# Kernel tuning notes

Hardware: AMD Instinct MI355X
Metric: run time of the kernel (lower is better)

Reference implementation:

```python
import jax, jax.numpy as jnp
import numpy as np
from jax import lax

N_T, N_CAPS, CAP_DIM = 8, 16, 16
EPS = 1e-6


def setup_inputs() -> dict:
    key = jax.random.key(0)
    k1, k2 = jax.random.split(key)
    B, H, W = 4, 64, 64
    C = N_T * N_CAPS * CAP_DIM  # 2048
    z = jax.random.normal(k1, (B, C, H, W), dtype=jnp.float32)
    u = jax.random.normal(k2, (B, C, H, W), dtype=jnp.float32)
    weight = jnp.ones((1, 1, 3, 3, 1), dtype=jnp.float32)  # Conv3d (O,I,kT,kD,kS), init ones
    beta = jnp.ones((1,), dtype=jnp.float32)  # correlated_mean_beta, mu_init=1.0
    return {"z": z, "u": u, "weight": weight, "beta": beta}


def reference(z, u, weight, beta):
    B, C, H, W = u.shape
    hw = H * W
    # (B, n_t, n_caps, cap_dim, hw) -> (B, n_caps, n_t, cap_dim, hw) -> (B*n_caps, 1, n_t, cap_dim, hw)
    u_caps = u.reshape(B, N_T, N_CAPS, CAP_DIM, hw)
    u_caps = jnp.transpose(u_caps, (0, 2, 1, 3, 4))
    u_caps = u_caps.reshape(-1, 1, N_T, CAP_DIM, hw)
    u_sq = u_caps * u_caps
    # circular pad over transform and cap_dim axes to keep 'same' size with 3x3x1 kernel
    padded = jnp.pad(u_sq, ((0, 0), (0, 0), (1, 1), (1, 1), (0, 0)), mode="wrap")
    v = lax.conv_general_dilated(
        padded, weight, window_strides=(1, 1, 1), padding="VALID",
        dimension_numbers=("NCDHW", "OIDHW", "NCDHW"),
    )  # (B*n_caps, 1, n_t, cap_dim, hw)
    v = v.reshape(B, N_CAPS, N_T, CAP_DIM, hw)
    v = jnp.transpose(v, (0, 2, 1, 3, 4)).reshape(z.shape)
    std = lax.rsqrt(v + EPS)
    s = (z + beta) * std
    return s
```

## Files before the change

kernel.cpp:

```cpp
#include <hip/hip_runtime.h>

#define N_T 8
#define N_CAPS 16
#define CAP_DIM 16
#define HW 4096
#define PT 256
#define NT 4
#define EPS 1e-6f

__global__ __launch_bounds__(512, 2) void caps_norm_kernel(
    const float* __restrict__ z, const float* __restrict__ u,
    const float* __restrict__ w, const float* __restrict__ beta,
    float* __restrict__ out)
{
    __shared__ float lds[128 * PT];

    const int tid = threadIdx.x;
    const int bid = blockIdx.x;
    const int pg  = bid & 3;
    const int c   = (bid >> 2) & 15;
    const int b   = bid >> 6;
    const int pbase = pg * (PT * NT);

    float W9[9];
#pragma unroll
    for (int i = 0; i < 9; ++i) W9[i] = w[i];
    const float bet = beta[0];

    const size_t base_b = (size_t)b * 2048 * HW;
    const float* ub = u + base_b;
    const float* zb = z + base_b;
    float*       ob = out + base_b;

    const int wv = tid >> 6;
    const int q  = tid & 63;

    int OFF[16];
#pragma unroll
    for (int k = 0; k < 16; ++k) {
        int r = wv + (k << 3);
        int t = r >> 4, d = r & 15;
        OFF[k] = (t * 256 + c * 16 + d) * HW + (q << 2);
    }

    float4 uA[16], uB[16];

#define STAGE_U(TI, UR)                                                      \
    {                                                                        \
        const int p0_ = pbase + (TI) * PT;                                   \
        _Pragma("unroll")                                                    \
        for (int k = 0; k < 16; ++k)                                         \
            UR[k] = *(const float4*)(ub + OFF[k] + p0_);                     \
    }

#define SQW(UR)                                                              \
    {                                                                        \
        _Pragma("unroll")                                                    \
        for (int k = 0; k < 16; ++k) {                                       \
            float4 v = UR[k];                                                \
            float4 sq;                                                       \
            sq.x = v.x*v.x; sq.y = v.y*v.y; sq.z = v.z*v.z; sq.w = v.w*v.w;  \
            *(float4*)(&lds[((wv + (k << 3)) << 8) + (q << 2)]) = sq;        \
        }                                                                    \
    }

#define COMP(TI)                                                             \
    {                                                                        \
        const int p0_ = pbase + (TI) * PT;                                   \
        _Pragma("unroll")                                                    \
        for (int k = 0; k < 16; ++k) {                                       \
            int r = wv + (k << 3);                                           \
            int t = r >> 4, d = r & 15;                                      \
            float ax = 0.f, ay = 0.f, az = 0.f, aw = 0.f;                    \
            _Pragma("unroll")                                                \
            for (int i = 0; i < 3; ++i) {                                    \
                int tt = (t + i + 7) & 7;                                    \
                _Pragma("unroll")                                            \
                for (int j = 0; j < 3; ++j) {                                \
                    int dd = (d + j + 15) & 15;                              \
                    float ww = W9[i * 3 + j];                                \
                    const float4 a = *(const float4*)(                       \
                        &lds[(((tt << 4) + dd) << 8) + (q << 2)]);           \
                    ax += ww*a.x; ay += ww*a.y; az += ww*a.z; aw += ww*a.w;  \
                }                                                            \
            }                                                                \
            const float4 z4 = *(const float4*)(zb + OFF[k] + p0_);           \
            float4 o;                                                        \
            o.x = (z4.x + bet) * rsqrtf(ax + EPS);                           \
            o.y = (z4.y + bet) * rsqrtf(ay + EPS);                           \
            o.z = (z4.z + bet) * rsqrtf(az + EPS);                           \
            o.w = (z4.w + bet) * rsqrtf(aw + EPS);                           \
            *(float4*)(ob + OFF[k] + p0_) = o;                               \
        }                                                                    \
    }

    STAGE_U(0, uA)
    SQW(uA)
    __syncthreads();

    STAGE_U(1, uB)
    COMP(0)
    __syncthreads();
    SQW(uB)
    __syncthreads();

    STAGE_U(2, uA)
    COMP(1)
    __syncthreads();
    SQW(uA)
    __syncthreads();

    STAGE_U(3, uB)
    COMP(2)
    __syncthreads();
    SQW(uB)
    __syncthreads();

    COMP(3)

#undef STAGE_U
#undef SQW
#undef COMP
}

extern "C" void kernel_launch(void* const* d_in, const int* in_sizes, int n_in,
                              void* d_out, int out_size, void* d_ws, size_t ws_size,
                              hipStream_t stream) {
    const float* z    = (const float*)d_in[0];
    const float* u    = (const float*)d_in[1];
    const float* w    = (const float*)d_in[2];
    const float* beta = (const float*)d_in[3];
    float* out = (float*)d_out;

    caps_norm_kernel<<<dim3(256), dim3(512), 0, stream>>>(z, u, w, beta, out);
}
```

Baseline: 349.1 us.

## Single-buffer u staging and remap thread-to-channel assignment for load and compute

Replaces the double register buffers with one staging array, issuing the next tile's u loads right after the LDS write so they overlap the barrier and compute. The staging load now gives each wave 16 consecutive channel rows, and compute uses a different mapping where each wave covers 4 rows by 16 float4 columns. Launch bounds drop from 2 blocks to 1 per SM, which allows more registers per thread but may reduce occupancy. Coalescing changes: global accesses become 256-byte segments per row instead of 1 KB per row.

New measurement: 338.4 us. -3.1%, faster.

```diff
diff --git a/kernel.cpp b/kernel.cpp
--- a/kernel.cpp
+++ b/kernel.cpp
@@ -1,14 +1,11 @@
 #include <hip/hip_runtime.h>
 
-#define N_T 8
-#define N_CAPS 16
-#define CAP_DIM 16
 #define HW 4096
 #define PT 256
 #define NT 4
 #define EPS 1e-6f
 
-__global__ __launch_bounds__(512, 2) void caps_norm_kernel(
+__global__ __launch_bounds__(512, 1) void caps_norm_kernel(
     const float* __restrict__ z, const float* __restrict__ u,
     const float* __restrict__ w, const float* __restrict__ beta,
     float* __restrict__ out)
@@ -16,11 +13,13 @@
     __shared__ float lds[128 * PT];
 
     const int tid = threadIdx.x;
+    const int wv  = tid >> 6;
+    const int ln  = tid & 63;
     const int bid = blockIdx.x;
     const int pg  = bid & 3;
     const int c   = (bid >> 2) & 15;
     const int b   = bid >> 6;
-    const int pbase = pg * (PT * NT);
+    const int pblk = pg * (PT * NT);
 
     float W9[9];
 #pragma unroll
@@ -32,94 +31,90 @@
     const float* zb = z + base_b;
     float*       ob = out + base_b;
 
-    const int wv = tid >> 6;
-    const int q  = tid & 63;
+    float4 uS[16];
 
-    int OFF[16];
-#pragma unroll
-    for (int k = 0; k < 16; ++k) {
-        int r = wv + (k << 3);
-        int t = r >> 4, d = r & 15;
-        OFF[k] = (t * 256 + c * 16 + d) * HW + (q << 2);
+#define STAGE(T)                                                              \
+    {                                                                         \
+        const int p0_ = pblk + (T) * PT;                                      \
+        _Pragma("unroll")                                                     \
+        for (int k = 0; k < 16; ++k) {                                        \
+            const int r = wv * 16 + k;                                        \
+            const int ch = (r >> 4) * 256 + c * 16 + (r & 15);                \
+            uS[k] = *(const float4*)(ub + (size_t)ch * HW + p0_ + ln * 4);    \
+        }                                                                     \
     }
 
-    float4 uA[16], uB[16];
-
-#define STAGE_U(TI, UR)                                                      \
-    {                                                                        \
-        const int p0_ = pbase + (TI) * PT;                                   \
-        _Pragma("unroll")                                                    \
-        for (int k = 0; k < 16; ++k)                                         \
-            UR[k] = *(const float4*)(ub + OFF[k] + p0_);                     \
+#define SQWRITE()                                                             \
+    {                                                                         \
+        _Pragma("unroll")                                                     \
+        for (int k = 0; k < 16; ++k) {                                        \
+            const int r = wv * 16 + k;                                        \
+            const float4 v = uS[k];                                           \
+            float4 s4;                                                        \
+            s4.x = v.x*v.x; s4.y = v.y*v.y; s4.z = v.z*v.z; s4.w = v.w*v.w;   \
+            *(float4*)(&lds[r * PT + ln * 4]) = s4;                           \
+        }                                                                     \
     }
 
-#define SQW(UR)                                                              \
-    {                                                                        \
-        _Pragma("unroll")                                                    \
-        for (int k = 0; k < 16; ++k) {                                       \
-            float4 v = UR[k];                                                \
-            float4 sq;                                                       \
-            sq.x = v.x*v.x; sq.y = v.y*v.y; sq.z = v.z*v.z; sq.w = v.w*v.w;  \
-            *(float4*)(&lds[((wv + (k << 3)) << 8) + (q << 2)]) = sq;        \
-        }                                                                    \
+#define COMP(T)                                                               \
+    {                                                                         \
+        const int p0_ = pblk + (T) * PT;                                      \
+        _Pragma("unroll")                                                     \
+        for (int k = 0; k < 16; ++k) {                                        \
+            const int r = (wv + 8 * (k >> 2)) * 4 + (ln >> 4);                \
+            const int q = (k & 3) * 16 + (ln & 15);                           \
+            const int t = r >> 4, d = r & 15;                                 \
+            const int ch = t * 256 + c * 16 + d;                              \
+            const size_t g = (size_t)ch * HW + p0_ + q * 4;                   \
+            const float4 z4 = *(const float4*)(zb + g);                       \
+            float ax = 0.f, ay = 0.f, az_ = 0.f, aw = 0.f;                    \
+            _Pragma("unroll")                                                 \
+            for (int i = 0; i < 3; ++i) {                                     \
+                const int tt = (t + i + 7) & 7;                               \
+                _Pragma("unroll")                                             \
+                for (int j = 0; j < 3; ++j) {                                 \
+                    const int dd = (d + j + 15) & 15;                         \
+                    const float ww = W9[i * 3 + j];                           \
+                    const float4 a = *(const float4*)(                        \
+                        &lds[((tt << 4) + dd) * PT + q * 4]);                 \
+                    ax += ww*a.x; ay += ww*a.y; az_ += ww*a.z; aw += ww*a.w;  \
+                }                                                             \
+            }                                                                 \
+            float4 o;                                                         \
+            o.x = (z4.x + bet) * rsqrtf(ax + EPS);                            \
+            o.y = (z4.y + bet) * rsqrtf(ay + EPS);                            \
+            o.z = (z4.z + bet) * rsqrtf(az_ + EPS);                           \
+            o.w = (z4.w + bet) * rsqrtf(aw + EPS);                            \
+            *(float4*)(ob + g) = o;                                           \
+        }                                                                     \
     }
 
-#define COMP(TI)                                                             \
-    {                                                                        \
-        const int p0_ = pbase + (TI) * PT;                                   \
-        _Pragma("unroll")                                                    \
-        for (int k = 0; k < 16; ++k) {                                       \
-            int r = wv + (k << 3);                                           \
-            int t = r >> 4, d = r & 15;                                      \
-            float ax = 0.f, ay = 0.f, az = 0.f, aw = 0.f;                    \
-            _Pragma("unroll")                                                \
-            for (int i = 0; i < 3; ++i) {                                    \
-                int tt = (t + i + 7) & 7;                                    \
-                _Pragma("unroll")                                            \
-                for (int j = 0; j < 3; ++j) {                                \
-                    int dd = (d + j + 15) & 15;                              \
-                    float ww = W9[i * 3 + j];                                \
-                    const float4 a = *(const float4*)(                       \
-                        &lds[(((tt << 4) + dd) << 8) + (q << 2)]);           \
-                    ax += ww*a.x; ay += ww*a.y; az += ww*a.z; aw += ww*a.w;  \
-                }                                                            \
-            }                                                                \
-            const float4 z4 = *(const float4*)(zb + OFF[k] + p0_);           \
-            float4 o;                                                        \
-            o.x = (z4.x + bet) * rsqrtf(ax + EPS);                           \
-            o.y = (z4.y + bet) * rsqrtf(ay + EPS);                           \
-            o.z = (z4.z + bet) * rsqrtf(az + EPS);                           \
-            o.w = (z4.w + bet) * rsqrtf(aw + EPS);                           \
-            *(float4*)(ob + OFF[k] + p0_) = o;                               \
-        }                                                                    \
-    }
-
-    STAGE_U(0, uA)
-    SQW(uA)
+    STAGE(0)
+    SQWRITE()
+    STAGE(1)
     __syncthreads();
 
-    STAGE_U(1, uB)
     COMP(0)
     __syncthreads();
-    SQW(uB)
+    SQWRITE()
+    STAGE(2)
     __syncthreads();
 
-    STAGE_U(2, uA)
     COMP(1)
     __syncthreads();
-    SQW(uA)
+    SQWRITE()
+    STAGE(3)
     __syncthreads();
 
-    STAGE_U(3, uB)
     COMP(2)
     __syncthreads();
-    SQW(uB)
+    SQWRITE()
     __syncthreads();
 
     COMP(3)
 
-#undef STAGE_U
-#undef SQW
+#undef STAGE
+#undef SQWRITE
 #undef COMP
 }
 
```
